# Performance work log

Hardware: AMD Instinct MI355X
Metric: run time of the kernel (lower is better)

## Reference

```python
import jax, jax.numpy as jnp
import numpy as np

N_NODES = 50000
N_EDGES = 800000
HC = 64      # hidden_channels
NG = 5       # num_gaussians
NF = 64      # num_filters
SL = 20      # short_len
NC = 2       # n_conv
Z_DIM = 2 * NF + SL  # 148
BN_EPS = 1e-5


def setup_inputs() -> dict:
    key = jax.random.key(0)
    ks = jax.random.split(key, 16)
    s = 0.05
    return {
        "h": jax.random.normal(ks[0], (N_NODES, HC), dtype=jnp.float32),
        "edge_index": jax.random.randint(ks[1], (2, N_EDGES), 0, N_NODES, dtype=jnp.int32),
        "edge_weight": jax.random.uniform(ks[2], (N_EDGES,), dtype=jnp.float32),
        "edge_attr": jax.random.uniform(ks[3], (N_EDGES, NG), dtype=jnp.float32),
        "lin0_w": jax.random.normal(ks[4], (HC, NF), dtype=jnp.float32) * s,
        "lin0_b": jnp.zeros((NF,), dtype=jnp.float32),
        "short_w": jax.random.normal(ks[5], (NG, SL), dtype=jnp.float32) * s,
        "short_b": jnp.zeros((SL,), dtype=jnp.float32),
        "linf_w": jax.random.normal(ks[6], (NC, Z_DIM, NF), dtype=jnp.float32) * s,
        "linf_b": jnp.zeros((NC, NF), dtype=jnp.float32),
        "lins_w": jax.random.normal(ks[7], (NC, Z_DIM, NF), dtype=jnp.float32) * s,
        "lins_b": jnp.zeros((NC, NF), dtype=jnp.float32),
        "bn_gamma": jnp.ones((NC, NF), dtype=jnp.float32),
        "bn_beta": jnp.zeros((NC, NF), dtype=jnp.float32),
        "data": 0,
    }


def reference(h, edge_index, edge_weight, edge_attr,
              lin0_w, lin0_b, short_w, short_b,
              linf_w, linf_b, lins_w, lins_b,
              bn_gamma, bn_beta, data):
    # lin0 + relu
    out = jax.nn.relu(h @ lin0_w + lin0_b)                      # [N, NF]
    # short edge-attr projection + relu
    ea = jax.nn.relu(edge_attr @ short_w + short_b)             # [E, SL]
    src = edge_index[0]  # x_j (source)
    dst = edge_index[1]  # x_i (target / aggregation index)
    n = out.shape[0]
    for l in range(NC):
        x_i = out[dst]                                          # [E, NF]
        x_j = out[src]                                          # [E, NF]
        z = jnp.concatenate([x_i, x_j, ea], axis=-1)            # [E, 148]
        msg = jax.nn.sigmoid(z @ linf_w[l] + linf_b[l]) * \
              jax.nn.softplus(z @ lins_w[l] + lins_b[l])        # [E, NF]
        agg = jax.ops.segment_sum(msg, dst, num_segments=n)     # [N, NF]
        # BatchNorm1d (training-mode batch stats, biased variance)
        mean = jnp.mean(agg, axis=0)
        var = jnp.mean((agg - mean) ** 2, axis=0)
        bn = (agg - mean) * jax.lax.rsqrt(var + BN_EPS) * bn_gamma[l] + bn_beta[l]
        conv_out = bn + out                                     # CGConv internal residual
        out = out + jax.nn.relu(conv_out)                       # _Interactions residual
    return out
```

## Files before the change

### kernel.cpp

```cpp
#include <hip/hip_runtime.h>
#include <hip/hip_bf16.h>

#define N_NODES 50000
#define N_EDGES 800000
#define NBK 391
#define EPW 20
#define EW_BLOCKS 10000

typedef __hip_bfloat16 bf16;
typedef unsigned int u32;
typedef unsigned short u16;
typedef _Float16 hh2 __attribute__((ext_vector_type(2)));

#if defined(__has_builtin)
#if __has_builtin(__builtin_amdgcn_fdot2)
#define HAVE_FDOT2 1
#endif
#endif

__device__ __forceinline__ float bfb(u32 b) { return __uint_as_float(b << 16); }

__device__ __forceinline__ u16 f2bf(float x) {
    bf16 a = __float2bfloat16(x);
    u16 u;
    __builtin_memcpy(&u, &a, 2);
    return u;
}

__device__ __forceinline__ hh2 pkrtz(float a, float b) {
    auto r = __builtin_amdgcn_cvt_pkrtz(a, b);
    hh2 o;
    __builtin_memcpy(&o, &r, 4);
    return o;
}

__device__ __forceinline__ float ldf(const void* p, long i, int f32) {
    if (f32) return ((const float*)p)[i];
    return bfb((u32)((const u16*)p)[i]);
}

__device__ __forceinline__ int detect_f32(const u32* g) { return g[0] == 0x3F800000u; }

__global__ __launch_bounds__(256) void k_front(const void* __restrict__ h,
        const void* __restrict__ w, const void* __restrict__ b,
        const u32* __restrict__ gr, u16* __restrict__ outw,
        const int* __restrict__ ei, u32* __restrict__ bmat,
        uint4* __restrict__ aggz4,
        const void* __restrict__ eattr, const void* __restrict__ short_w,
        const void* __restrict__ short_b, u32* __restrict__ sea_e) {
    int t = threadIdx.x;
    uint4 z4 = {0u, 0u, 0u, 0u};
    for (int i = blockIdx.x * 256 + t; i < N_NODES * 16; i += 1536 * 256)
        aggz4[i] = z4;
    int f32 = detect_f32(gr);
    if (blockIdx.x >= 1024) {
        __shared__ float swl[100];
        __shared__ float sbl[20];
        if (t < 100) swl[t] = ldf(short_w, t, f32);
        if (t < 20) sbl[t] = ldf(short_b, t, f32);
        __syncthreads();
        int bid = blockIdx.x - 1024;
        for (int e = bid * 256 + t; e < N_EDGES; e += 512 * 256) {
            float a0 = ldf(eattr, (long)e * 5 + 0, f32);
            float a1 = ldf(eattr, (long)e * 5 + 1, f32);
            float a2 = ldf(eattr, (long)e * 5 + 2, f32);
            float a3 = ldf(eattr, (long)e * 5 + 3, f32);
            float a4 = ldf(eattr, (long)e * 5 + 4, f32);
            u32 buf[10];
            #pragma unroll
            for (int j = 0; j < 10; ++j) {
                float e0 = sbl[2 * j], e1 = sbl[2 * j + 1];
                e0 = fmaf(a0, swl[0 * 20 + 2 * j], e0);
                e1 = fmaf(a0, swl[0 * 20 + 2 * j + 1], e1);
                e0 = fmaf(a1, swl[1 * 20 + 2 * j], e0);
                e1 = fmaf(a1, swl[1 * 20 + 2 * j + 1], e1);
                e0 = fmaf(a2, swl[2 * 20 + 2 * j], e0);
                e1 = fmaf(a2, swl[2 * 20 + 2 * j + 1], e1);
                e0 = fmaf(a3, swl[3 * 20 + 2 * j], e0);
                e1 = fmaf(a3, swl[3 * 20 + 2 * j + 1], e1);
                e0 = fmaf(a4, swl[4 * 20 + 2 * j], e0);
                e1 = fmaf(a4, swl[4 * 20 + 2 * j + 1], e1);
                e0 = fmaxf(e0, 0.f);
                e1 = fmaxf(e1, 0.f);
                hh2 h2 = pkrtz(e0, e1);
                u32 u;
                __builtin_memcpy(&u, &h2, 4);
                buf[j] = u;
            }
            u32* sp = sea_e + (size_t)e * 10u;
            #pragma unroll
            for (int q = 0; q < 5; ++q) {
                uint2 v2 = {buf[2 * q], buf[2 * q + 1]};
                *(uint2*)(sp + 2 * q) = v2;
            }
        }
        return;
    }
    if (blockIdx.x >= 512) {
        __shared__ int bcnt[NBK];
        for (int k = t; k < NBK; k += 256) bcnt[k] = 0;
        __syncthreads();
        int bid = blockIdx.x - 512;
        for (int e = bid * 256 + t; e < N_EDGES; e += 512 * 256) {
            int dst = ei[N_EDGES + e];
            atomicAdd(&bcnt[dst >> 7], 1);
        }
        __syncthreads();
        for (int k = t; k < NBK; k += 256)
            bmat[(size_t)k * 512 + bid] = (u32)bcnt[k];
        return;
    }
    __shared__ float Wl[64 * 64];
    __shared__ float bl[64];
    __shared__ float hs[16 * 64];
    for (int i = t; i < 4096; i += 256) Wl[i] = ldf(w, i, f32);
    if (t < 64) bl[t] = ldf(b, t, f32);
    int c = t & 63, g = t >> 6;
    for (int chunk = blockIdx.x; chunk < N_NODES / 16; chunk += 512) {
        __syncthreads();
        int node0 = chunk * 16;
        for (int i = t; i < 1024; i += 256) hs[i] = ldf(h, (long)node0 * 64 + i, f32);
        __syncthreads();
        #pragma unroll
        for (int nn = 0; nn < 4; ++nn) {
            int n = g * 4 + nn;
            float acc = bl[c];
            #pragma unroll
            for (int k = 0; k < 64; ++k) acc = fmaf(hs[n * 64 + k], Wl[k * 64 + c], acc);
            outw[(node0 + n) * 64 + c] = f2bf(fmaxf(acc, 0.f));
        }
    }
}

__global__ __launch_bounds__(512) void k_scan(u32* __restrict__ bmat,
        u32* __restrict__ total) {
    __shared__ int wsum[8];
    int t = threadIdx.x, lane = t & 63, wv = t >> 6;
    int bk = blockIdx.x;
    int v = (int)bmat[(size_t)bk * 512 + t];
    int incl = v;
    #pragma unroll
    for (int d = 1; d < 64; d <<= 1) {
        int x = __shfl_up(incl, d, 64);
        if (lane >= d) incl += x;
    }
    if (lane == 63) wsum[wv] = incl;
    __syncthreads();
    if (wv == 0) {
        int s = (lane < 8) ? wsum[lane] : 0;
        int si = s;
        #pragma unroll
        for (int d = 1; d < 8; d <<= 1) {
            int x = __shfl_up(si, d, 64);
            if (lane >= d) si += x;
        }
        if (lane < 8) wsum[lane] = si - s;
    }
    __syncthreads();
    int excl = incl - v + wsum[wv];
    bmat[(size_t)bk * 512 + t] = (u32)excl;
    if (t == 511) total[bk] = (u32)(excl + v);
}

__global__ __launch_bounds__(512) void k_scan2(const u32* __restrict__ total,
        u32* __restrict__ bucketbase) {
    __shared__ int wsum[8];
    int t = threadIdx.x, lane = t & 63, wv = t >> 6;
    int v = (t < NBK) ? (int)total[t] : 0;
    int incl = v;
    #pragma unroll
    for (int d = 1; d < 64; d <<= 1) {
        int x = __shfl_up(incl, d, 64);
        if (lane >= d) incl += x;
    }
    if (lane == 63) wsum[wv] = incl;
    __syncthreads();
    if (wv == 0) {
        int s = (lane < 8) ? wsum[lane] : 0;
        int si = s;
        #pragma unroll
        for (int d = 1; d < 8; d <<= 1) {
            int x = __shfl_up(si, d, 64);
            if (lane >= d) si += x;
        }
        if (lane < 8) wsum[lane] = si - s;
    }
    __syncthreads();
    if (t < NBK) bucketbase[t] = (u32)(incl - v + wsum[wv]);
    if (t == 0) bucketbase[NBK] = N_EDGES;
}

__global__ __launch_bounds__(256) void k_pproj_bin(const u16* __restrict__ outw,
        const void* __restrict__ linf_w, const void* __restrict__ lins_w,
        const void* __restrict__ linf_b, const void* __restrict__ lins_b,
        const u32* __restrict__ gr, bf16* __restrict__ P,
        const int* __restrict__ ei, const u32* __restrict__ bmat,
        const u32* __restrict__ bucketbase, uint2* __restrict__ tmp,
        u32* __restrict__ wpk) {
    int t = threadIdx.x;
    int f32 = detect_f32(gr);
    if (blockIdx.x >= 512) {
        if (blockIdx.x == 512 && t < 128) {
            int ly = t >> 6, ln = t & 63;
            long wb = (long)ly * 9472 + 8192;
            u32* wp = wpk + (size_t)(ly * 64 + ln) * 20;
            #pragma unroll
            for (int j = 0; j < 10; ++j) {
                hh2 fp = pkrtz(ldf(linf_w, wb + (2 * j) * 64 + ln, f32),
                               ldf(linf_w, wb + (2 * j + 1) * 64 + ln, f32));
                hh2 sp = pkrtz(ldf(lins_w, wb + (2 * j) * 64 + ln, f32),
                               ldf(lins_w, wb + (2 * j + 1) * 64 + ln, f32));
                u32 uf, us;
                __builtin_memcpy(&uf, &fp, 4);
                __builtin_memcpy(&us, &sp, 4);
                wp[2 * j] = uf;
                wp[2 * j + 1] = us;
            }
        }
        __shared__ u32 run[NBK];
        int bid = blockIdx.x - 512;
        for (int k = t; k < NBK; k += 256)
            run[k] = bucketbase[k] + bmat[(size_t)k * 512 + bid];
        __syncthreads();
        for (int e = bid * 256 + t; e < N_EDGES; e += 512 * 256) {
            int dst = ei[N_EDGES + e];
            int src = ei[e];
            u32 off = atomicAdd(&run[dst >> 7], 1u);
            uint2 v;
            v.x = ((u32)dst << 16) | (u32)src;
            v.y = (u32)e;
            tmp[off] = v;
        }
        return;
    }
    int b = t >> 6, c = t & 63;
    const void* wmat = (b < 2) ? linf_w : lins_w;
    long woff = (long)(b & 1) * 4096;
    float bias = 0.f;
    if (b == 0) bias = ldf(linf_b, c, f32);
    if (b == 2) bias = ldf(lins_b, c, f32);
    float wc[64];
    #pragma unroll
    for (int k = 0; k < 64; ++k) wc[k] = ldf(wmat, woff + k * 64 + c, f32);
    int stidx = (b & 1) * 128 + 2 * c + (b >> 1);
    __shared__ float hs[16 * 64];
    for (int chunk = blockIdx.x; chunk < N_NODES / 16; chunk += 512) {
        __syncthreads();
        int node0 = chunk * 16;
        {
            ushort4 hv = *(const ushort4*)(outw + (size_t)node0 * 64 + t * 4);
            hs[t * 4 + 0] = bfb((u32)hv.x);
            hs[t * 4 + 1] = bfb((u32)hv.y);
            hs[t * 4 + 2] = bfb((u32)hv.z);
            hs[t * 4 + 3] = bfb((u32)hv.w);
        }
        __syncthreads();
        for (int n = 0; n < 16; ++n) {
            float acc = bias;
            #pragma unroll
            for (int k = 0; k < 64; ++k) acc = fmaf(hs[n * 64 + k], wc[k], acc);
            P[(size_t)(node0 + n) * 256 + stidx] = __float2bfloat16(acc);
        }
    }
}

__global__ __launch_bounds__(256) void k_bin2(const uint2* __restrict__ tmp,
        const u32* __restrict__ bucketbase, uint2* __restrict__ bb) {
    __shared__ int hist[128];
    __shared__ u32 run[128];
    __shared__ int wpart[2];
    int t = threadIdx.x;
    int bk = blockIdx.x;
    u32 lo = bucketbase[bk], hi = bucketbase[bk + 1];
    if (t < 128) hist[t] = 0;
    __syncthreads();
    for (u32 i = lo + t; i < hi; i += 256) {
        u32 pk = tmp[i].x;
        atomicAdd(&hist[(pk >> 16) & 127], 1);
    }
    __syncthreads();
    int v_ = 0, incl_ = 0;
    if (t < 128) {
        int lane = t & 63;
        v_ = hist[t];
        incl_ = v_;
        #pragma unroll
        for (int d = 1; d < 64; d <<= 1) {
            int x = __shfl_up(incl_, d, 64);
            if (lane >= d) incl_ += x;
        }
        if (lane == 63) wpart[t >> 6] = incl_;
    }
    __syncthreads();
    if (t < 128) {
        int add = (t >= 64) ? wpart[0] : 0;
        run[t] = lo + (u32)(incl_ - v_ + add);
    }
    __syncthreads();
    for (u32 i = lo + t; i < hi; i += 256) {
        uint2 v = tmp[i];
        u32 slot = atomicAdd(&run[(v.x >> 16) & 127], 1u);
        bb[slot] = v;
    }
}

struct EB { u32 ea; u32 pd[4]; u32 ps[4]; int d[4]; };

__global__ __launch_bounds__(256) void k_edge_flat(const uint2* __restrict__ bb,
        const u32* __restrict__ sea_e, const u32* __restrict__ wpk, int layer,
        const u32* __restrict__ Pw, float* __restrict__ agg) {
    int t = threadIdx.x, lane = t & 63, wv = t >> 6;
    int wid = blockIdx.x * 4 + wv;
    int base = wid * EPW;

    int eo = (lane / 10) & 3, j10 = lane % 10;
    const uint4* wv4 = (const uint4*)(wpk + (size_t)(layer * 64 + lane) * 20);
    uint4 q0 = wv4[0], q1 = wv4[1], q2 = wv4[2], q3 = wv4[3], q4 = wv4[4];
    u32 wbuf[20] = {q0.x, q0.y, q0.z, q0.w, q1.x, q1.y, q1.z, q1.w,
                    q2.x, q2.y, q2.z, q2.w, q3.x, q3.y, q3.z, q3.w,
                    q4.x, q4.y, q4.z, q4.w};
    hh2 wf2[10], ws2[10];
    #pragma unroll
    for (int j = 0; j < 10; ++j) {
        __builtin_memcpy(&wf2[j], &wbuf[2 * j], 4);
        __builtin_memcpy(&ws2[j], &wbuf[2 * j + 1], 4);
    }

    float acc = 0.f;
    int cur = -1;

    auto issueA = [&](uint2& A, int b) {
        A = bb[(u32)base + 4u * (u32)b + ((u32)lane & 3u)];
    };
    auto issueB = [&](EB& B, uint2 A, int b) {
        u32 eid = (u32)__shfl((int)A.y, eo, 64);
        B.ea = sea_e[eid * 10u + (u32)j10];
        #pragma unroll
        for (int i = 0; i < 4; ++i) {
            u32 pki = (u32)__builtin_amdgcn_readlane((int)A.x, i);
            int d = (int)(pki >> 16);
            u32 s = pki & 0xFFFFu;
            B.d[i] = d;
            B.pd[i] = Pw[(u32)d * 128u + (u32)lane];
            B.ps[i] = Pw[s * 128u + 64u + (u32)lane];
        }
    };
    auto computeC = [&](const EB& B) {
        #pragma unroll
        for (int i = 0; i < 4; ++i) {
            int d = B.d[i];
            u32 pd = B.pd[i], ps = B.ps[i];
            float f = bfb(pd & 0xFFFFu) + bfb(ps & 0xFFFFu);
            float s = __uint_as_float(pd & 0xFFFF0000u) +
                      __uint_as_float(ps & 0xFFFF0000u);
            #pragma unroll
            for (int j = 0; j < 10; ++j) {
                u32 u = (u32)__builtin_amdgcn_readlane((int)B.ea, 10 * i + j);
                hh2 hu;
                __builtin_memcpy(&hu, &u, 4);
#ifdef HAVE_FDOT2
                f = __builtin_amdgcn_fdot2(hu, wf2[j], f, false);
                s = __builtin_amdgcn_fdot2(hu, ws2[j], s, false);
#else
                f = fmaf((float)hu[0], (float)wf2[j][0], f);
                f = fmaf((float)hu[1], (float)wf2[j][1], f);
                s = fmaf((float)hu[0], (float)ws2[j][0], s);
                s = fmaf((float)hu[1], (float)ws2[j][1], s);
#endif
            }
            float sig = 1.f / (1.f + __expf(-f));
            float sp = fmaxf(s, 0.f) + __logf(1.f + __expf(-fabsf(s)));
            if (d != cur) {
                if (cur >= 0)
                    atomicAdd(agg + (u32)cur * 64u + (u32)lane, acc);
                acc = 0.f;
                cur = d;
            }
            acc += sig * sp;
        }
    };

    uint2 A0, A1, A2, A3;
    EB B0, B1, B2, B3;
    issueA(A0, 0); issueA(A1, 1); issueA(A2, 2); issueA(A3, 3);
    issueB(B0, A0, 0); issueB(B1, A1, 1); issueB(B2, A2, 2);
    issueA(A0, 4);
    issueB(B3, A3, 3);
    computeC(B0);
    issueB(B0, A0, 4);
    computeC(B1);
    computeC(B2);
    computeC(B3);
    computeC(B0);
    if (cur >= 0) atomicAdd(agg + (u32)cur * 64u + (u32)lane, acc);
}

__global__ __launch_bounds__(256) void k_stats(const float* __restrict__ aggf,
        float* __restrict__ stats) {
    int t = threadIdx.x;
    int r = t >> 4, c4 = (t & 15) * 4;
    float s0 = 0.f, s1 = 0.f, s2 = 0.f, s3 = 0.f;
    float q0 = 0.f, q1 = 0.f, q2 = 0.f, q3 = 0.f;
    for (int row = blockIdx.x * 16 + r; row < N_NODES; row += 256 * 16) {
        float4 v = *(const float4*)(aggf + (size_t)row * 64 + c4);
        s0 += v.x; s1 += v.y; s2 += v.z; s3 += v.w;
        q0 = fmaf(v.x, v.x, q0); q1 = fmaf(v.y, v.y, q1);
        q2 = fmaf(v.z, v.z, q2); q3 = fmaf(v.w, v.w, q3);
    }
    __shared__ float red[2][16][64];
    red[0][r][c4 + 0] = s0; red[0][r][c4 + 1] = s1;
    red[0][r][c4 + 2] = s2; red[0][r][c4 + 3] = s3;
    red[1][r][c4 + 0] = q0; red[1][r][c4 + 1] = q1;
    red[1][r][c4 + 2] = q2; red[1][r][c4 + 3] = q3;
    __syncthreads();
    if (t < 128) {
        int m = t >> 6, c = t & 63;
        float a = 0.f;
        #pragma unroll
        for (int k = 0; k < 16; ++k) a += red[m][k][c];
        atomicAdd(&stats[m * 64 + c], a);
    }
}

__global__ __launch_bounds__(256) void k_apply_pproj(float* __restrict__ aggf,
        const float* __restrict__ stats, const void* __restrict__ gamma,
        const void* __restrict__ beta, const u32* __restrict__ gr,
        u16* __restrict__ outw,
        const void* __restrict__ linf_w, const void* __restrict__ lins_w,
        const void* __restrict__ linf_b, const void* __restrict__ lins_b,
        bf16* __restrict__ P) {
    int f32 = detect_f32(gr);
    int t = threadIdx.x;
    int b = t >> 6, c = t & 63;
    int nid = t >> 4, c4 = (t & 15) * 4;
    const float invN = 1.f / (float)N_NODES;
    float m4[4], iv4[4], g4[4], b4[4];
    #pragma unroll
    for (int k = 0; k < 4; ++k) {
        float mean = stats[c4 + k] * invN;
        float var = fmaxf(stats[64 + c4 + k] * invN - mean * mean, 0.f);
        m4[k] = mean;
        iv4[k] = rsqrtf(var + 1e-5f);
        g4[k] = ldf(gamma, c4 + k, f32);
        b4[k] = ldf(beta, c4 + k, f32);
    }
    const void* wmat = (b < 2) ? linf_w : lins_w;
    long woff = 9472 + (long)(b & 1) * 4096;
    float bias = 0.f;
    if (b == 0) bias = ldf(linf_b, 64 + c, f32);
    if (b == 2) bias = ldf(lins_b, 64 + c, f32);
    float wc[64];
    #pragma unroll
    for (int k = 0; k < 64; ++k) wc[k] = ldf(wmat, woff + k * 64 + c, f32);
    int stidx = (b & 1) * 128 + 2 * c + (b >> 1);
    __shared__ float hs[16 * 64];
    for (int chunk = blockIdx.x; chunk < N_NODES / 16; chunk += 512) {
        __syncthreads();
        int node0 = chunk * 16;
        {
            size_t idx = (size_t)(node0 + nid) * 64 + c4;
            float4 a = *(const float4*)(aggf + idx);
            ushort4 ow = *(const ushort4*)(outw + idx);
            const float* ap = (const float*)&a;
            const u16* op = (const u16*)&ow;
            float no[4];
            #pragma unroll
            for (int k = 0; k < 4; ++k) {
                float o = bfb((u32)op[k]);
                float bn = fmaf((ap[k] - m4[k]) * iv4[k], g4[k], b4[k]);
                no[k] = o + fmaxf(bn + o, 0.f);
            }
            ushort4 nw = {f2bf(no[0]), f2bf(no[1]), f2bf(no[2]), f2bf(no[3])};
            *(ushort4*)(outw + idx) = nw;
            float4 z4 = {0.f, 0.f, 0.f, 0.f};
            *(float4*)(aggf + idx) = z4;
            float4 hv = {no[0], no[1], no[2], no[3]};
            *(float4*)(&hs[nid * 64 + c4]) = hv;
        }
        __syncthreads();
        for (int n = 0; n < 16; ++n) {
            float acc = bias;
            #pragma unroll
            for (int k = 0; k < 64; ++k) acc = fmaf(hs[n * 64 + k], wc[k], acc);
            P[(size_t)(node0 + n) * 256 + stidx] = __float2bfloat16(acc);
        }
    }
}

__global__ __launch_bounds__(256) void k_apply_final(const float* __restrict__ aggf,
        const float* __restrict__ stats, const void* __restrict__ gamma,
        const void* __restrict__ beta, const u32* __restrict__ gr,
        const u16* __restrict__ outw, void* __restrict__ dout) {
    int f32 = detect_f32(gr);
    const float invN = 1.f / (float)N_NODES;
    int t0 = blockIdx.x * 256 + threadIdx.x;
    int c4 = (t0 & 15) * 4;
    float m4[4], iv4[4], g4[4], b4[4];
    #pragma unroll
    for (int k = 0; k < 4; ++k) {
        float mean = stats[c4 + k] * invN;
        float var = fmaxf(stats[64 + c4 + k] * invN - mean * mean, 0.f);
        m4[k] = mean;
        iv4[k] = rsqrtf(var + 1e-5f);
        g4[k] = ldf(gamma, 64 + c4 + k, f32);
        b4[k] = ldf(beta, 64 + c4 + k, f32);
    }
    for (int i4 = t0; i4 < N_NODES * 16; i4 += 1024 * 256) {
        float4 a = *(const float4*)(aggf + (size_t)i4 * 4);
        ushort4 ow = *(const ushort4*)(outw + (size_t)i4 * 4);
        const float* ap = (const float*)&a;
        const u16* op = (const u16*)&ow;
        float no[4];
        #pragma unroll
        for (int k = 0; k < 4; ++k) {
            float o = bfb((u32)op[k]);
            float bn = fmaf((ap[k] - m4[k]) * iv4[k], g4[k], b4[k]);
            no[k] = o + fmaxf(bn + o, 0.f);
        }
        if (f32) {
            float4 o4 = {no[0], no[1], no[2], no[3]};
            *(float4*)((float*)dout + (size_t)i4 * 4) = o4;
        } else {
            ushort4 o4 = {f2bf(no[0]), f2bf(no[1]), f2bf(no[2]), f2bf(no[3])};
            *(ushort4*)((u16*)dout + (size_t)i4 * 4) = o4;
        }
    }
}

extern "C" void kernel_launch(void* const* d_in, const int* in_sizes, int n_in,
                              void* d_out, int out_size, void* d_ws, size_t ws_size,
                              hipStream_t stream) {
    const void* h       = d_in[0];
    const int*  ei      = (const int*)d_in[1];
    const void* eattr   = d_in[3];
    const void* lin0_w  = d_in[4];
    const void* lin0_b  = d_in[5];
    const void* short_w = d_in[6];
    const void* short_b = d_in[7];
    const void* linf_w  = d_in[8];
    const void* linf_b  = d_in[9];
    const void* lins_w  = d_in[10];
    const void* lins_b  = d_in[11];
    const void* gamma   = d_in[12];
    const void* beta    = d_in[13];
    const u32*  gr      = (const u32*)gamma;

    u16*   outw  = (u16*)d_ws;
    bf16*  P     = (bf16*)(outw + (size_t)N_NODES * 64);
    uint2* bb    = (uint2*)(P + (size_t)N_NODES * 256);
    float* aggf  = (float*)(bb + N_EDGES);
    float* stats = (float*)(aggf + (size_t)N_NODES * 64);
    u32*   bmat  = (u32*)(stats + 256);
    u32*   total = bmat + (size_t)NBK * 512;
    u32*   bucketbase = total + 400;
    u32*   sea_e = bucketbase + 400;
    u32*   wpk   = sea_e + (size_t)N_EDGES * 10;
    uint2* tmp   = (uint2*)(wpk + 2 * 64 * 20);

    (void)hipMemsetAsync(stats, 0, 256 * 4, stream);

    k_front<<<1536, 256, 0, stream>>>(h, lin0_w, lin0_b, gr, outw, ei, bmat,
                                      (uint4*)aggf, eattr, short_w, short_b,
                                      sea_e);
    k_scan<<<NBK, 512, 0, stream>>>(bmat, total);
    k_scan2<<<1, 512, 0, stream>>>(total, bucketbase);
    k_pproj_bin<<<1024, 256, 0, stream>>>(outw, linf_w, lins_w, linf_b, lins_b,
                                          gr, P, ei, bmat, bucketbase, tmp, wpk);
    k_bin2<<<NBK, 256, 0, stream>>>(tmp, bucketbase, bb);
    k_edge_flat<<<EW_BLOCKS, 256, 0, stream>>>(bb, sea_e, wpk, 0,
                                               (const u32*)P, aggf);
    k_stats<<<256, 256, 0, stream>>>(aggf, stats);
    k_apply_pproj<<<512, 256, 0, stream>>>(aggf, stats, gamma, beta, gr, outw,
                                           linf_w, lins_w, linf_b, lins_b, P);
    k_edge_flat<<<EW_BLOCKS, 256, 0, stream>>>(bb, sea_e, wpk, 1,
                                               (const u32*)P, aggf);
    k_stats<<<256, 256, 0, stream>>>(aggf, stats + 128);
    k_apply_final<<<1024, 256, 0, stream>>>(aggf, stats + 128, gamma, beta, gr,
                                            outw, d_out);
}
```

Measured before the change: 388.6 us.

## Compute edge-attr projection in binning kernel, store in sorted edge order

```diff
diff --git a/kernel.cpp b/kernel.cpp
--- a/kernel.cpp
+++ b/kernel.cpp
@@ -45,57 +45,12 @@
         const void* __restrict__ w, const void* __restrict__ b,
         const u32* __restrict__ gr, u16* __restrict__ outw,
         const int* __restrict__ ei, u32* __restrict__ bmat,
-        uint4* __restrict__ aggz4,
-        const void* __restrict__ eattr, const void* __restrict__ short_w,
-        const void* __restrict__ short_b, u32* __restrict__ sea_e) {
+        uint4* __restrict__ aggz4) {
     int t = threadIdx.x;
     uint4 z4 = {0u, 0u, 0u, 0u};
-    for (int i = blockIdx.x * 256 + t; i < N_NODES * 16; i += 1536 * 256)
+    for (int i = blockIdx.x * 256 + t; i < N_NODES * 16; i += 1024 * 256)
         aggz4[i] = z4;
     int f32 = detect_f32(gr);
-    if (blockIdx.x >= 1024) {
-        __shared__ float swl[100];
-        __shared__ float sbl[20];
-        if (t < 100) swl[t] = ldf(short_w, t, f32);
-        if (t < 20) sbl[t] = ldf(short_b, t, f32);
-        __syncthreads();
-        int bid = blockIdx.x - 1024;
-        for (int e = bid * 256 + t; e < N_EDGES; e += 512 * 256) {
-            float a0 = ldf(eattr, (long)e * 5 + 0, f32);
-            float a1 = ldf(eattr, (long)e * 5 + 1, f32);
-            float a2 = ldf(eattr, (long)e * 5 + 2, f32);
-            float a3 = ldf(eattr, (long)e * 5 + 3, f32);
-            float a4 = ldf(eattr, (long)e * 5 + 4, f32);
-            u32 buf[10];
-            #pragma unroll
-            for (int j = 0; j < 10; ++j) {
-                float e0 = sbl[2 * j], e1 = sbl[2 * j + 1];
-                e0 = fmaf(a0, swl[0 * 20 + 2 * j], e0);
-                e1 = fmaf(a0, swl[0 * 20 + 2 * j + 1], e1);
-                e0 = fmaf(a1, swl[1 * 20 + 2 * j], e0);
-                e1 = fmaf(a1, swl[1 * 20 + 2 * j + 1], e1);
-                e0 = fmaf(a2, swl[2 * 20 + 2 * j], e0);
-                e1 = fmaf(a2, swl[2 * 20 + 2 * j + 1], e1);
-                e0 = fmaf(a3, swl[3 * 20 + 2 * j], e0);
-                e1 = fmaf(a3, swl[3 * 20 + 2 * j + 1], e1);
-                e0 = fmaf(a4, swl[4 * 20 + 2 * j], e0);
-                e1 = fmaf(a4, swl[4 * 20 + 2 * j + 1], e1);
-                e0 = fmaxf(e0, 0.f);
-                e1 = fmaxf(e1, 0.f);
-                hh2 h2 = pkrtz(e0, e1);
-                u32 u;
-                __builtin_memcpy(&u, &h2, 4);
-                buf[j] = u;
-            }
-            u32* sp = sea_e + (size_t)e * 10u;
-            #pragma unroll
-            for (int q = 0; q < 5; ++q) {
-                uint2 v2 = {buf[2 * q], buf[2 * q + 1]};
-                *(uint2*)(sp + 2 * q) = v2;
-            }
-        }
-        return;
-    }
     if (blockIdx.x >= 512) {
         __shared__ int bcnt[NBK];
         for (int k = t; k < NBK; k += 256) bcnt[k] = 0;
@@ -265,11 +220,19 @@
 }
 
 __global__ __launch_bounds__(256) void k_bin2(const uint2* __restrict__ tmp,
-        const u32* __restrict__ bucketbase, uint2* __restrict__ bb) {
+        const u32* __restrict__ bucketbase, u32* __restrict__ pk_arr,
+        const void* __restrict__ eattr, const void* __restrict__ short_w,
+        const void* __restrict__ short_b, const u32* __restrict__ gr,
+        u32* __restrict__ sea_s) {
     __shared__ int hist[128];
     __shared__ u32 run[128];
     __shared__ int wpart[2];
+    __shared__ float swl[100];
+    __shared__ float sbl[20];
     int t = threadIdx.x;
+    int f32 = detect_f32(gr);
+    if (t < 100) swl[t] = ldf(short_w, t, f32);
+    if (t < 20) sbl[t] = ldf(short_b, t, f32);
     int bk = blockIdx.x;
     u32 lo = bucketbase[bk], hi = bucketbase[bk + 1];
     if (t < 128) hist[t] = 0;
@@ -300,20 +263,54 @@
     for (u32 i = lo + t; i < hi; i += 256) {
         uint2 v = tmp[i];
         u32 slot = atomicAdd(&run[(v.x >> 16) & 127], 1u);
-        bb[slot] = v;
+        pk_arr[slot] = v.x;
+        u32 eid = v.y;
+        float a0 = ldf(eattr, (long)eid * 5 + 0, f32);
+        float a1 = ldf(eattr, (long)eid * 5 + 1, f32);
+        float a2 = ldf(eattr, (long)eid * 5 + 2, f32);
+        float a3 = ldf(eattr, (long)eid * 5 + 3, f32);
+        float a4 = ldf(eattr, (long)eid * 5 + 4, f32);
+        u32 buf[10];
+        #pragma unroll
+        for (int j = 0; j < 10; ++j) {
+            float e0 = sbl[2 * j], e1 = sbl[2 * j + 1];
+            e0 = fmaf(a0, swl[0 * 20 + 2 * j], e0);
+            e1 = fmaf(a0, swl[0 * 20 + 2 * j + 1], e1);
+            e0 = fmaf(a1, swl[1 * 20 + 2 * j], e0);
+            e1 = fmaf(a1, swl[1 * 20 + 2 * j + 1], e1);
+            e0 = fmaf(a2, swl[2 * 20 + 2 * j], e0);
+            e1 = fmaf(a2, swl[2 * 20 + 2 * j + 1], e1);
+            e0 = fmaf(a3, swl[3 * 20 + 2 * j], e0);
+            e1 = fmaf(a3, swl[3 * 20 + 2 * j + 1], e1);
+            e0 = fmaf(a4, swl[4 * 20 + 2 * j], e0);
+            e1 = fmaf(a4, swl[4 * 20 + 2 * j + 1], e1);
+            e0 = fmaxf(e0, 0.f);
+            e1 = fmaxf(e1, 0.f);
+            hh2 h2 = pkrtz(e0, e1);
+            u32 u;
+            __builtin_memcpy(&u, &h2, 4);
+            buf[j] = u;
+        }
+        u32* sp = sea_s + (size_t)slot * 10u;
+        #pragma unroll
+        for (int q = 0; q < 5; ++q) {
+            uint2 v2 = {buf[2 * q], buf[2 * q + 1]};
+            *(uint2*)(sp + 2 * q) = v2;
+        }
     }
 }
 
 struct EB { u32 ea; u32 pd[4]; u32 ps[4]; int d[4]; };
 
-__global__ __launch_bounds__(256) void k_edge_flat(const uint2* __restrict__ bb,
-        const u32* __restrict__ sea_e, const u32* __restrict__ wpk, int layer,
+__global__ __launch_bounds__(256) void k_edge_flat(const u32* __restrict__ pk_arr,
+        const u32* __restrict__ sea_s, const u32* __restrict__ wpk, int layer,
         const u32* __restrict__ Pw, float* __restrict__ agg) {
     int t = threadIdx.x, lane = t & 63, wv = t >> 6;
     int wid = blockIdx.x * 4 + wv;
     int base = wid * EPW;
 
     int eo = (lane / 10) & 3, j10 = lane % 10;
+    int seaoff = eo * 10 + j10;
     const uint4* wv4 = (const uint4*)(wpk + (size_t)(layer * 64 + lane) * 20);
     uint4 q0 = wv4[0], q1 = wv4[1], q2 = wv4[2], q3 = wv4[3], q4 = wv4[4];
     u32 wbuf[20] = {q0.x, q0.y, q0.z, q0.w, q1.x, q1.y, q1.z, q1.w,
@@ -329,15 +326,14 @@
     float acc = 0.f;
     int cur = -1;
 
-    auto issueA = [&](uint2& A, int b) {
-        A = bb[(u32)base + 4u * (u32)b + ((u32)lane & 3u)];
+    auto issueA = [&](u32& Apk, int b) {
+        Apk = pk_arr[(u32)base + 4u * (u32)b + ((u32)lane & 3u)];
     };
-    auto issueB = [&](EB& B, uint2 A, int b) {
-        u32 eid = (u32)__shfl((int)A.y, eo, 64);
-        B.ea = sea_e[eid * 10u + (u32)j10];
+    auto issueB = [&](EB& B, u32 Apk, int b) {
+        B.ea = sea_s[(u32)(base + 4 * b) * 10u + (u32)seaoff];
         #pragma unroll
         for (int i = 0; i < 4; ++i) {
-            u32 pki = (u32)__builtin_amdgcn_readlane((int)A.x, i);
+            u32 pki = (u32)__builtin_amdgcn_readlane((int)Apk, i);
             int d = (int)(pki >> 16);
             u32 s = pki & 0xFFFFu;
             B.d[i] = d;
@@ -380,7 +376,7 @@
         }
     };
 
-    uint2 A0, A1, A2, A3;
+    u32 A0, A1, A2, A3;
     EB B0, B1, B2, B3;
     issueA(A0, 0); issueA(A1, 1); issueA(A2, 2); issueA(A3, 3);
     issueB(B0, A0, 0); issueB(B1, A1, 1); issueB(B2, A2, 2);
@@ -547,32 +543,32 @@
 
     u16*   outw  = (u16*)d_ws;
     bf16*  P     = (bf16*)(outw + (size_t)N_NODES * 64);
-    uint2* bb    = (uint2*)(P + (size_t)N_NODES * 256);
-    float* aggf  = (float*)(bb + N_EDGES);
+    u32*   pk_arr = (u32*)(P + (size_t)N_NODES * 256);
+    float* aggf  = (float*)(pk_arr + N_EDGES);
     float* stats = (float*)(aggf + (size_t)N_NODES * 64);
     u32*   bmat  = (u32*)(stats + 256);
     u32*   total = bmat + (size_t)NBK * 512;
     u32*   bucketbase = total + 400;
-    u32*   sea_e = bucketbase + 400;
-    u32*   wpk   = sea_e + (size_t)N_EDGES * 10;
+    u32*   sea_s = bucketbase + 400;
+    u32*   wpk   = sea_s + (size_t)N_EDGES * 10;
     uint2* tmp   = (uint2*)(wpk + 2 * 64 * 20);
 
     (void)hipMemsetAsync(stats, 0, 256 * 4, stream);
 
-    k_front<<<1536, 256, 0, stream>>>(h, lin0_w, lin0_b, gr, outw, ei, bmat,
-                                      (uint4*)aggf, eattr, short_w, short_b,
-                                      sea_e);
+    k_front<<<1024, 256, 0, stream>>>(h, lin0_w, lin0_b, gr, outw, ei, bmat,
+                                      (uint4*)aggf);
     k_scan<<<NBK, 512, 0, stream>>>(bmat, total);
     k_scan2<<<1, 512, 0, stream>>>(total, bucketbase);
     k_pproj_bin<<<1024, 256, 0, stream>>>(outw, linf_w, lins_w, linf_b, lins_b,
                                           gr, P, ei, bmat, bucketbase, tmp, wpk);
-    k_bin2<<<NBK, 256, 0, stream>>>(tmp, bucketbase, bb);
-    k_edge_flat<<<EW_BLOCKS, 256, 0, stream>>>(bb, sea_e, wpk, 0,
+    k_bin2<<<NBK, 256, 0, stream>>>(tmp, bucketbase, pk_arr, eattr, short_w,
+                                    short_b, gr, sea_s);
+    k_edge_flat<<<EW_BLOCKS, 256, 0, stream>>>(pk_arr, sea_s, wpk, 0,
                                                (const u32*)P, aggf);
     k_stats<<<256, 256, 0, stream>>>(aggf, stats);
     k_apply_pproj<<<512, 256, 0, stream>>>(aggf, stats, gamma, beta, gr, outw,
                                            linf_w, lins_w, linf_b, lins_b, P);
-    k_edge_flat<<<EW_BLOCKS, 256, 0, stream>>>(bb, sea_e, wpk, 1,
+    k_edge_flat<<<EW_BLOCKS, 256, 0, stream>>>(pk_arr, sea_s, wpk, 1,
                                                (const u32*)P, aggf);
     k_stats<<<256, 256, 0, stream>>>(aggf, stats + 128);
     k_apply_final<<<1024, 256, 0, stream>>>(aggf, stats + 128, gamma, beta, gr,
```

Result: slower. 408.7 us (+5.2%).
